# Kernel optimization log

Measured on AMD Instinct MI355X. Metric: run time of the kernel, lower is better.

Reference implementation:

```python
import jax, jax.numpy as jnp
import numpy as np


def force_fn(x):
    # Harmonic force F = -grad U, U(x) = 0.5 * ||x||^2 (Ornstein-Uhlenbeck).
    return -x


def setup_inputs() -> dict:
    key = jax.random.key(0)
    x0 = jax.random.normal(key, (100000, 3), dtype=jnp.float32)
    return {
        "x0": x0,
        "gamma": jnp.ones((1,), dtype=jnp.float32),
        "kT": jnp.ones((1,), dtype=jnp.float32),
        "dt": jnp.ones((1,), dtype=jnp.float32) * 0.01,
        "n_steps": 1000,
        "store_every": 10,
    }


def reference(x0, gamma, kT, dt, n_steps, store_every):
    # Overdamped Langevin: x_{t+1} = x_t + F(x_t)/gamma * dt + sqrt(2*kT*dt/gamma) * N(0, I)
    gamma_s = gamma.reshape(())
    kT_s = kT.reshape(())
    dt_s = dt.reshape(())
    noise_scale = jnp.sqrt(2.0 * kT_s * dt_s / gamma_s)

    n_chunks = n_steps // store_every  # trajectory stored every `store_every` steps
    keys = jax.random.split(jax.random.key(42), n_chunks * store_every)
    keys = keys.reshape((n_chunks, store_every))

    def step(x, k):
        noise = jax.random.normal(k, x.shape, x.dtype)
        x_new = x + force_fn(x) / gamma_s * dt_s + noise_scale * noise
        return x_new, None

    def chunk(x, ks):
        x, _ = jax.lax.scan(step, x, ks)
        return x, x  # carry and store the state after each chunk

    _, traj = jax.lax.scan(chunk, x0, keys)  # (n_chunks, N, 3)
    return jnp.concatenate([x0[None], traj], axis=0)  # (n_chunks + 1, N, 3)
```

## Files before the change

kernel.cpp:

```cpp
#include <hip/hip_runtime.h>


#define KCAP 1024

#if __has_builtin(__builtin_amdgcn_alignbit)
#define ROTL(x, r) __builtin_amdgcn_alignbit((x), (x), 32u - (r))
#define SPLICE(bits) __builtin_amdgcn_alignbit(0x7Fu, (bits), 9u)
#else
#define ROTL(x, r) __builtin_rotateleft32((x), (r))
#define SPLICE(bits) (((bits) >> 9) | 0x3f800000u)
#endif

struct alignas(16) Rec { unsigned s, b, c, a; };
struct KTable { Rec r[KCAP]; };

constexpr unsigned crotl(unsigned v, int r) { return (v << r) | (v >> (32 - r)); }

constexpr KTable gen_keys() {
    KTable t{};
    for (unsigned j = 0; j < KCAP; ++j) {
        const unsigned k0 = 0u, k1 = 42u, ks2 = k0 ^ k1 ^ 0x1BD11BDAu;
        unsigned x0 = 0u + k0, x1 = j + k1;
        const int rots[20] = {13,15,26,6, 17,29,16,24, 13,15,26,6, 17,29,16,24, 13,15,26,6};
        int ri = 0;
        for (int blk = 0; blk < 5; ++blk) {
            for (int rr = 0; rr < 4; ++rr) { x0 += x1; x1 = crotl(x1, rots[ri++]); x1 ^= x0; }
            switch (blk) {
                case 0: x0 += k1;  x1 += ks2 + 1u; break;
                case 1: x0 += ks2; x1 += k0 + 2u;  break;
                case 2: x0 += k0;  x1 += k1 + 3u;  break;
                case 3: x0 += k1;  x1 += ks2 + 4u; break;
                case 4: x0 += ks2; x1 += k0 + 5u;  break;
            }
        }
        const unsigned b0 = x0, b1 = x1;
        t.r[j] = Rec{b0 + b1, b1, b0 ^ b1 ^ 0x1BD11BDAu, b0};
    }
    return t;
}

__constant__ KTable KTAB = gen_keys();

struct Consts {
    float P0, P1, P2, P3, P4, P5, P6, P7, P8;
    float NLN2, M25, M3, LO;
};

__device__ __forceinline__ float poly_lo(float w, const Consts& cc) {
    float p = cc.P0;
    p = fmaf(p, w, cc.P1);
    p = fmaf(p, w, cc.P2);
    p = fmaf(p, w, cc.P3);
    p = fmaf(p, w, cc.P4);
    p = fmaf(p, w, cc.P5);
    p = fmaf(p, w, cc.P6);
    p = fmaf(p, w, cc.P7);
    p = fmaf(p, w, cc.P8);
    return p;
}
__device__ __forceinline__ float poly_hi(float s) {
    float p =       -0.000200214257f;
    p = fmaf(p, s,   0.000100950558f);
    p = fmaf(p, s,   0.00134934322f);
    p = fmaf(p, s,  -0.00367342844f);
    p = fmaf(p, s,   0.00573950773f);
    p = fmaf(p, s,  -0.0076224613f);
    p = fmaf(p, s,   0.00943887047f);
    p = fmaf(p, s,   1.00167406f);
    p = fmaf(p, s,   2.83297682f);
    return p;
}

__device__ __forceinline__ float normal_of(Rec k, unsigned t, const Consts& cc) {
    unsigned x0 = k.s + t;
    unsigned x1 = ROTL(k.b + t, 13) ^ x0;
#define RND(r) { x0 += x1; x1 = ROTL(x1, r) ^ x0; }
    RND(15) RND(26) RND(6)
    x0 += k.b; x1 += k.c + 1u;
    RND(17) RND(29) RND(16) RND(24)
    x0 += k.c; x1 += k.a + 2u;
    RND(13) RND(15) RND(26) RND(6)
    x0 += k.a; x1 += k.b + 3u;
    RND(17) RND(29) RND(16) RND(24)
    x0 += k.b; x1 += k.c + 4u;
    RND(13) RND(15) RND(26) RND(6)
    x0 += k.c; x1 += k.a + 5u;
#undef RND
    unsigned bits = x0 ^ x1;

    float F = __uint_as_float(SPLICE(bits));
    float u = fmaf(F, 2.0f, cc.M3);
    u = fmaxf(u, cc.LO);
    float h = fmaf(-u, u, 1.0f);
    float l2 = __log2f(h);
    float p;
    if (__builtin_expect(__any(l2 <= -7.2134752f), 0)) {
        float w  = l2 * cc.NLN2;
        float p1 = poly_lo(w + cc.M25, cc);
        float p2 = poly_hi(sqrtf(w) + cc.M3);
        p = (l2 > -7.2134752f) ? p1 : p2;
    } else {
        p = poly_lo(fmaf(l2, cc.NLN2, cc.M25), cc);
    }
    return p * u;
}

__device__ __forceinline__ Rec make_key(unsigned j) {
    const unsigned k0 = 0u, k1 = 42u, ks2 = k0 ^ k1 ^ 0x1BD11BDAu;
    unsigned x0 = k0, x1 = j + k1;
#define RND(r) { x0 += x1; x1 = ROTL(x1, r) ^ x0; }
    RND(13) RND(15) RND(26) RND(6)
    x0 += k1;  x1 += ks2 + 1u;
    RND(17) RND(29) RND(16) RND(24)
    x0 += ks2; x1 += k0 + 2u;
    RND(13) RND(15) RND(26) RND(6)
    x0 += k0;  x1 += k1 + 3u;
    RND(17) RND(29) RND(16) RND(24)
    x0 += k1;  x1 += ks2 + 4u;
    RND(13) RND(15) RND(26) RND(6)
    x0 += ks2; x1 += k0 + 5u;
#undef RND
    Rec r; r.s = x0 + x1; r.b = x1; r.c = x0 ^ x1 ^ 0x1BD11BDAu; r.a = x0;
    return r;
}

__global__ __launch_bounds__(256) void OverdampedLangevin_62362925138458_kernel(
    const float* __restrict__ x0p,
    const float* __restrict__ gamma_p,
    const float* __restrict__ kT_p,
    const float* __restrict__ dt_p,
    const int*   __restrict__ nsteps_p,
    const int*   __restrict__ store_p,
    float*       __restrict__ out,
    int E)
{
    const int n_steps = *nsteps_p;
    const int store_every = *store_p;

    const unsigned t = blockIdx.x * blockDim.x + threadIdx.x;
    if ((int)t >= E) return;

    const float g  = gamma_p[0];
    const float kT = kT_p[0];
    const float dt = dt_p[0];
    float scale2 = sqrtf(2.0f * kT * dt / g) * 1.41421356f;
    float na = -(dt / g);

    Consts cc{2.81022636e-08f,  3.43273939e-07f, -3.5233877e-06f,
             -4.39150654e-06f,  0.00021858087f,  -0.00125372503f,
             -0.00417768164f,   0.246640727f,     1.50140941f,
             -0.69314718f,     -2.5f,            -3.0f, -0.99999994f};
    asm("" : "+v"(cc.P0), "+v"(cc.P1), "+v"(cc.P2), "+v"(cc.P3), "+v"(cc.P4),
             "+v"(cc.P5), "+v"(cc.P6), "+v"(cc.P7), "+v"(cc.P8),
             "+v"(cc.NLN2), "+v"(cc.M25), "+v"(cc.M3), "+v"(cc.LO),
             "+v"(scale2), "+v"(na));

    float x = x0p[t];
    out[t] = x;

    if (store_every == 10 && n_steps % 10 == 0 && n_steps <= KCAP) {
        const int nc = n_steps / 10;
        float* op = out + (size_t)E + t;
        int idx = 0;
        for (int c = 0; c < nc; ++c) {
#pragma unroll
            for (int s = 0; s < 10; ++s) {
                float z = normal_of(KTAB.r[idx + s], t, cc);
                x = fmaf(scale2, z, fmaf(na, x, x));
            }
            idx += 10;
            *op = x;
            op += (size_t)E;
        }
    } else {
        int frame = 1, since = 0;
#pragma unroll 1
        for (int s = 0; s < n_steps; ++s) {
            Rec k = (s < KCAP) ? KTAB.r[s] : make_key((unsigned)s);
            float z = normal_of(k, t, cc);
            x = fmaf(scale2, z, fmaf(na, x, x));
            if (++since == store_every) {
                since = 0;
                out[(size_t)frame * (size_t)E + t] = x;
                ++frame;
            }
        }
    }
}

extern "C" void kernel_launch(void* const* d_in, const int* in_sizes, int n_in,
                              void* d_out, int out_size, void* d_ws, size_t ws_size,
                              hipStream_t stream) {
    const float* x0    = (const float*)d_in[0];
    const float* gam   = (const float*)d_in[1];
    const float* kT    = (const float*)d_in[2];
    const float* dt    = (const float*)d_in[3];
    const int*   nst   = (const int*)d_in[4];
    const int*   sev   = (const int*)d_in[5];
    float*       out   = (float*)d_out;

    const int E = in_sizes[0];
    const int blocks = (E + 255) / 256;
    OverdampedLangevin_62362925138458_kernel<<<blocks, 256, 0, stream>>>(
        x0, gam, kT, dt, nst, sev, out, E);
}
```

Before: 708.1 us.

## Split Langevin into parallel per-chunk noise kernel and linear scan kernel

```diff
diff --git a/kernel.cpp b/kernel.cpp
--- a/kernel.cpp
+++ b/kernel.cpp
@@ -2,14 +2,6 @@
 
 
 #define KCAP 1024
-
-#if __has_builtin(__builtin_amdgcn_alignbit)
-#define ROTL(x, r) __builtin_amdgcn_alignbit((x), (x), 32u - (r))
-#define SPLICE(bits) __builtin_amdgcn_alignbit(0x7Fu, (bits), 9u)
-#else
-#define ROTL(x, r) __builtin_rotateleft32((x), (r))
-#define SPLICE(bits) (((bits) >> 9) | 0x3f800000u)
-#endif
 
 struct alignas(16) Rec { unsigned s, b, c, a; };
 struct KTable { Rec r[KCAP]; };
@@ -41,6 +33,14 @@
 
 __constant__ KTable KTAB = gen_keys();
 
+#if __has_builtin(__builtin_amdgcn_alignbit)
+#define ROTL(x, r) __builtin_amdgcn_alignbit((x), (x), 32u - (r))
+#define SPLICE(bits) __builtin_amdgcn_alignbit(0x7Fu, (bits), 9u)
+#else
+#define ROTL(x, r) __builtin_rotateleft32((x), (r))
+#define SPLICE(bits) (((bits) >> 9) | 0x3f800000u)
+#endif
+
 struct Consts {
     float P0, P1, P2, P3, P4, P5, P6, P7, P8;
     float NLN2, M25, M3, LO;
@@ -71,7 +71,7 @@
     return p;
 }
 
-__device__ __forceinline__ float normal_of(Rec k, unsigned t, const Consts& cc) {
+__device__ __forceinline__ unsigned tf_bits(Rec k, unsigned t) {
     unsigned x0 = k.s + t;
     unsigned x1 = ROTL(k.b + t, 13) ^ x0;
 #define RND(r) { x0 += x1; x1 = ROTL(x1, r) ^ x0; }
@@ -86,8 +86,10 @@
     RND(13) RND(15) RND(26) RND(6)
     x0 += k.c; x1 += k.a + 5u;
 #undef RND
-    unsigned bits = x0 ^ x1;
-
+    return x0 ^ x1;
+}
+
+__device__ __forceinline__ float normal_of_bits(unsigned bits, const Consts& cc) {
     float F = __uint_as_float(SPLICE(bits));
     float u = fmaf(F, 2.0f, cc.M3);
     u = fmaxf(u, cc.LO);
@@ -124,20 +126,94 @@
     return r;
 }
 
-__global__ __launch_bounds__(256) void OverdampedLangevin_62362925138458_kernel(
+__device__ __forceinline__ bool fast_ok(int se, int ns, int n_chunks) {
+    return se == 10 && n_chunks > 0 && ns / 10 == n_chunks && 10 * n_chunks <= KCAP;
+}
+
+__global__ __launch_bounds__(256) void langevin_noise(
+    const float* __restrict__ gamma_p, const float* __restrict__ kT_p,
+    const float* __restrict__ dt_p, const int* __restrict__ nsteps_p,
+    const int* __restrict__ store_p, float* __restrict__ out,
+    int E, int n_chunks)
+{
+    if (!fast_ok(*store_p, *nsteps_p, n_chunks)) return;
+    const unsigned e = blockIdx.x * 256 + threadIdx.x;
+    if ((int)e >= E) return;
+
+    const float g  = gamma_p[0];
+    const float kT = kT_p[0];
+    const float dt = dt_p[0];
+    float scale2 = sqrtf(2.0f * kT * dt / g) * 1.41421356f;
+    const float na = -(dt / g);
+    const float a  = 1.0f + na;
+
+    Consts cc{2.81022636e-08f,  3.43273939e-07f, -3.5233877e-06f,
+             -4.39150654e-06f,  0.00021858087f,  -0.00125372503f,
+             -0.00417768164f,   0.246640727f,     1.50140941f,
+             -0.69314718f,     -2.5f,            -3.0f, -0.99999994f};
+    asm("" : "+v"(cc.P0), "+v"(cc.P1), "+v"(cc.P2), "+v"(cc.P3), "+v"(cc.P4),
+             "+v"(cc.P5), "+v"(cc.P6), "+v"(cc.P7), "+v"(cc.P8),
+             "+v"(cc.NLN2), "+v"(cc.M25), "+v"(cc.M3), "+v"(cc.LO));
+
+    float w[10];
+    w[9] = scale2;
+#pragma unroll
+    for (int s = 8; s >= 0; --s) w[s] = w[s + 1] * a;
+
+    const int c0 = 2 * blockIdx.y;
+    const int c1 = c0 + 1;
+    const bool has1 = (c1 < n_chunks);
+
+    float S0 = 0.0f, S1 = 0.0f;
+#pragma unroll
+    for (int s = 0; s < 10; ++s) {
+        float z0 = normal_of_bits(tf_bits(KTAB.r[c0 * 10 + s], e), cc);
+        S0 = fmaf(w[s], z0, S0);
+        if (has1) {
+            float z1 = normal_of_bits(tf_bits(KTAB.r[c1 * 10 + s], e), cc);
+            S1 = fmaf(w[s], z1, S1);
+        }
+    }
+    out[(size_t)(c0 + 1) * (size_t)E + e] = S0;
+    if (has1) out[(size_t)(c1 + 1) * (size_t)E + e] = S1;
+}
+
+__global__ __launch_bounds__(256) void langevin_scan(
     const float* __restrict__ x0p,
-    const float* __restrict__ gamma_p,
-    const float* __restrict__ kT_p,
-    const float* __restrict__ dt_p,
-    const int*   __restrict__ nsteps_p,
-    const int*   __restrict__ store_p,
-    float*       __restrict__ out,
-    int E)
+    const int* __restrict__ nsteps_p, const int* __restrict__ store_p,
+    const float* __restrict__ gamma_p, const float* __restrict__ dt_p,
+    float* __restrict__ out, int E, int n_chunks)
 {
-    const int n_steps = *nsteps_p;
-    const int store_every = *store_p;
-
-    const unsigned t = blockIdx.x * blockDim.x + threadIdx.x;
+    if (!fast_ok(*store_p, *nsteps_p, n_chunks)) return;
+    const unsigned e = blockIdx.x * 256 + threadIdx.x;
+    if ((int)e >= E) return;
+
+    const float na = -(dt_p[0] / gamma_p[0]);
+    float x = x0p[e];
+    out[e] = x;
+    float* p = out + (size_t)E + e;
+#pragma unroll 2
+    for (int c = 0; c < n_chunks; ++c) {
+        float S = *p;
+#pragma unroll
+        for (int s = 0; s < 10; ++s) x = fmaf(na, x, x);
+        x += S;
+        *p = x;
+        p += (size_t)E;
+    }
+}
+
+__global__ __launch_bounds__(256) void langevin_generic(
+    const float* __restrict__ x0p,
+    const float* __restrict__ gamma_p, const float* __restrict__ kT_p,
+    const float* __restrict__ dt_p, const int* __restrict__ nsteps_p,
+    const int* __restrict__ store_p, float* __restrict__ out,
+    int E, int n_chunks)
+{
+    const int ns = *nsteps_p;
+    const int se = *store_p;
+    if (fast_ok(se, ns, n_chunks)) return;
+    const unsigned t = blockIdx.x * 256 + threadIdx.x;
     if ((int)t >= E) return;
 
     const float g  = gamma_p[0];
@@ -157,33 +233,17 @@
 
     float x = x0p[t];
     out[t] = x;
-
-    if (store_every == 10 && n_steps % 10 == 0 && n_steps <= KCAP) {
-        const int nc = n_steps / 10;
-        float* op = out + (size_t)E + t;
-        int idx = 0;
-        for (int c = 0; c < nc; ++c) {
-#pragma unroll
-            for (int s = 0; s < 10; ++s) {
-                float z = normal_of(KTAB.r[idx + s], t, cc);
-                x = fmaf(scale2, z, fmaf(na, x, x));
-            }
-            idx += 10;
-            *op = x;
-            op += (size_t)E;
-        }
-    } else {
-        int frame = 1, since = 0;
+    int frame = 1, since = 0;
 #pragma unroll 1
-        for (int s = 0; s < n_steps; ++s) {
-            Rec k = (s < KCAP) ? KTAB.r[s] : make_key((unsigned)s);
-            float z = normal_of(k, t, cc);
-            x = fmaf(scale2, z, fmaf(na, x, x));
-            if (++since == store_every) {
-                since = 0;
+    for (int s = 0; s < ns; ++s) {
+        Rec k = (s < KCAP) ? KTAB.r[s] : make_key((unsigned)s);
+        float z = normal_of_bits(tf_bits(k, t), cc);
+        x = fmaf(scale2, z, fmaf(na, x, x));
+        if (++since == se) {
+            since = 0;
+            if (frame <= n_chunks)
                 out[(size_t)frame * (size_t)E + t] = x;
-                ++frame;
-            }
+            ++frame;
         }
     }
 }
@@ -200,7 +260,16 @@
     float*       out   = (float*)d_out;
 
     const int E = in_sizes[0];
-    const int blocks = (E + 255) / 256;
-    OverdampedLangevin_62362925138458_kernel<<<blocks, 256, 0, stream>>>(
-        x0, gam, kT, dt, nst, sev, out, E);
-}
+    const int eb = (E + 255) / 256;
+    int n_chunks = (E > 0) ? (out_size / E - 1) : -1;
+    if (n_chunks < 1 || (size_t)(n_chunks + 1) * (size_t)E != (size_t)out_size)
+        n_chunks = -1;
+
+    langevin_generic<<<eb, 256, 0, stream>>>(x0, gam, kT, dt, nst, sev, out, E, n_chunks);
+
+    if (n_chunks >= 1) {
+        dim3 g1(eb, (n_chunks + 1) / 2);
+        langevin_noise<<<g1, 256, 0, stream>>>(gam, kT, dt, nst, sev, out, E, n_chunks);
+        langevin_scan<<<eb, 256, 0, stream>>>(x0, nst, sev, gam, dt, out, E, n_chunks);
+    }
+}
```

Result: faster. 658.0 us (-7.1%).
